# Optimization experiments

Measured on AMD Instinct MI355X. Metric: run time of the kernel, lower is better.

The kernel has to match this reference:

```python
import jax, jax.numpy as jnp
import numpy as np

N_NODES = 100000


def _gcn_conv(x, w, b, edge_index, n):
    # Linear transform
    x = x @ w + b
    # Add self loops
    loops = jnp.tile(jnp.arange(n, dtype=edge_index.dtype), (2, 1))
    ei = jnp.concatenate([edge_index, loops], axis=1)
    src, tgt = ei[0], ei[1]
    # Degree of source nodes (every node has a self loop -> deg >= 1)
    deg = jax.ops.segment_sum(jnp.ones(src.shape, x.dtype), src, num_segments=n)
    dinv = deg ** -0.5
    norm = dinv[src] * dinv[tgt]  # [E+N]
    # Gather-scale-scatter: out[t] += norm_e * x[s]
    msgs = norm[:, None] * x[src]  # [E+N, out_ch]
    return jax.ops.segment_sum(msgs, tgt, num_segments=n)


def setup_inputs() -> dict:
    key = jax.random.key(0)
    ks = jax.random.split(key, 6)
    n, f_in, hid, n_cls, e = N_NODES, 512, 16, 40, 3200000
    x = jax.random.normal(ks[0], (n, f_in), dtype=jnp.float32)
    edge_index = jax.random.randint(ks[1], (2, e), 0, n, dtype=jnp.int64)
    w1 = jax.random.normal(ks[2], (f_in, hid), dtype=jnp.float32) * (1.0 / np.sqrt(f_in))
    b1 = jax.random.normal(ks[3], (hid,), dtype=jnp.float32) * 0.01
    w2 = jax.random.normal(ks[4], (hid, n_cls), dtype=jnp.float32) * (1.0 / np.sqrt(hid))
    b2 = jax.random.normal(ks[5], (n_cls,), dtype=jnp.float32) * 0.01
    return {"x": x, "edge_index": edge_index, "w1": w1, "b1": b1, "w2": w2, "b2": b2}


def reference(x, edge_index, w1, b1, w2, b2):
    n = x.shape[0]
    h = _gcn_conv(x, w1, b1, edge_index, n)
    h = jax.nn.relu(h)
    # dropout is identity in eval mode (F.dropout with training=False)
    h = _gcn_conv(h, w2, b2, edge_index, n)
    return jax.nn.log_softmax(h, axis=1)
```

## Files before the change

### kernel.cpp

```cpp
#include <hip/hip_runtime.h>
#include <hip/hip_fp16.h>
#include <cstdint>

#define FIN 512
#define HID 16
#define NCLS 40
#define SHIFT 8
#define NBCAP 512
#define NBLK 512
#define BR 128
#define KC 32


__global__ void count_kernel(const int* __restrict__ ei, int E, int nb,
                             int* __restrict__ hist_src_g, int* __restrict__ hist_tgt_g) {
    __shared__ int hs[NBCAP], ht[NBCAP];
    for (int j = threadIdx.x; j < NBCAP; j += 256) { hs[j] = 0; ht[j] = 0; }
    __syncthreads();
    for (int i = blockIdx.x * 256 + threadIdx.x; i < E; i += NBLK * 256) {
        atomicAdd(&hs[ei[i] >> SHIFT], 1);
        atomicAdd(&ht[ei[E + i] >> SHIFT], 1);
    }
    __syncthreads();
    int base = blockIdx.x * NBCAP;
    for (int j = threadIdx.x; j < NBCAP; j += 256) {
        hist_src_g[base + j] = hs[j];
        hist_tgt_g[base + j] = ht[j];
    }
}


__global__ void colscan_kernel(int* __restrict__ hist_src_g, int* __restrict__ hist_tgt_g,
                               int* __restrict__ btot) {
    __shared__ int tmp[NBLK];
    int b = blockIdx.x;
    int* h = blockIdx.y ? hist_tgt_g : hist_src_g;
    int t = threadIdx.x;
    int v = h[t * NBCAP + b];
    tmp[t] = v;
    __syncthreads();
    for (int off = 1; off < NBLK; off <<= 1) {
        int a = (t >= off) ? tmp[t - off] : 0;
        __syncthreads();
        tmp[t] += a;
        __syncthreads();
    }
    h[t * NBCAP + b] = tmp[t] - v;
    if (t == NBLK - 1) btot[blockIdx.y * NBCAP + b] = tmp[NBLK - 1];
}


__global__ void bucketscan_kernel(const int* __restrict__ btot, int nb,
                                  int* __restrict__ src_base, int* __restrict__ tgt_base,
                                  int* __restrict__ row_ptr, int N, int E) {
    __shared__ int tmp[512];
    int t = threadIdx.x;
    int v = (t < nb) ? btot[t] : 0;
    tmp[t] = v;
    __syncthreads();
    for (int off = 1; off < 512; off <<= 1) {
        int a = (t >= off) ? tmp[t - off] : 0;
        __syncthreads();
        tmp[t] += a;
        __syncthreads();
    }
    if (t < nb) src_base[t] = tmp[t] - v;
    __syncthreads();
    int v2 = (t < nb) ? btot[NBCAP + t] : 0;
    tmp[t] = v2;
    __syncthreads();
    for (int off = 1; off < 512; off <<= 1) {
        int a = (t >= off) ? tmp[t - off] : 0;
        __syncthreads();
        tmp[t] += a;
        __syncthreads();
    }
    if (t < nb) tgt_base[t] = tmp[t] - v2;
    if (t == 0) { src_base[nb] = E; tgt_base[nb] = E; row_ptr[N] = E; }
}


__global__ void scatter_kernel(const int* __restrict__ ei, int E, int nb,
                               const int* __restrict__ hist_src_g,
                               const int* __restrict__ hist_tgt_g,
                               const int* __restrict__ src_base,
                               const int* __restrict__ tgt_base,
                               unsigned char* __restrict__ tmp_src,
                               unsigned int* __restrict__ tmp_tgt) {
    __shared__ int cs[NBCAP], ct[NBCAP];
    int blk = blockIdx.x;
    for (int j = threadIdx.x; j < nb; j += 256) {
        cs[j] = src_base[j] + hist_src_g[blk * NBCAP + j];
        ct[j] = tgt_base[j] + hist_tgt_g[blk * NBCAP + j];
    }
    __syncthreads();
    for (int i = blk * 256 + threadIdx.x; i < E; i += NBLK * 256) {
        int s = ei[i], tg = ei[E + i];
        int ps = atomicAdd(&cs[s >> SHIFT], 1);
        tmp_src[ps] = (unsigned char)(s & 255);
        int pt = atomicAdd(&ct[tg >> SHIFT], 1);
        tmp_tgt[pt] = ((unsigned int)(tg & 255) << 17) | (unsigned int)s;
    }
}


__global__ void finedeg_kernel(const unsigned char* __restrict__ tmp_src,
                               const int* __restrict__ src_base,
                               float* __restrict__ dinv, int N) {
    __shared__ int hist[256];
    int b = blockIdx.x;
    int t = threadIdx.x;
    hist[t] = 0;
    __syncthreads();
    int beg = src_base[b], end = src_base[b + 1];
    for (int i = beg + t; i < end; i += 256)
        atomicAdd(&hist[tmp_src[i]], 1);
    __syncthreads();
    int node = b * 256 + t;
    if (node < N) dinv[node] = rsqrtf((float)(hist[t] + 1));
}


__global__ void finecsr_kernel(const unsigned int* __restrict__ tmp_tgt,
                               const int* __restrict__ tgt_base,
                               const float* __restrict__ dinv,
                               int* __restrict__ row_ptr, int* __restrict__ edges,
                               __half* __restrict__ edinv, int N) {
    __shared__ int hist[256];
    __shared__ int scan[256];
    int b = blockIdx.x;
    int t = threadIdx.x;
    hist[t] = 0;
    __syncthreads();
    int beg = tgt_base[b], end = tgt_base[b + 1];
    for (int i = beg + t; i < end; i += 256)
        atomicAdd(&hist[tmp_tgt[i] >> 17], 1);
    __syncthreads();
    int v = hist[t];
    scan[t] = v;
    __syncthreads();
    for (int off = 1; off < 256; off <<= 1) {
        int a = (t >= off) ? scan[t - off] : 0;
        __syncthreads();
        scan[t] += a;
        __syncthreads();
    }
    int ex = scan[t] - v;
    int node = b * 256 + t;
    if (node < N) row_ptr[node] = beg + ex;
    hist[t] = ex;
    __syncthreads();
    for (int i = beg + t; i < end; i += 256) {
        unsigned int w = tmp_tgt[i];
        int tl = (int)(w >> 17);
        int src = (int)(w & 0x1FFFF);
        int pos = beg + atomicAdd(&hist[tl], 1);
        edges[pos] = src;
        edinv[pos] = __float2half(dinv[src]);
    }
}


__global__ void linear1_kernel(const float* __restrict__ x, const float* __restrict__ w1,
                               const float* __restrict__ b1, __half* __restrict__ h1h, int n) {
    __shared__ float xs[KC][BR + 2];
    __shared__ float wsc[KC * HID];
    __shared__ float bl[HID];
    int t = threadIdx.x;
    if (t < HID) bl[t] = b1[t];
    int row0 = blockIdx.x * BR;
    int rp = t >> 2;
    int cq = (t & 3) * 4;
    float acc0[4] = {0, 0, 0, 0};
    float acc1[4] = {0, 0, 0, 0};

    float4 xp[4];
    float wp[2];
    int rr_[4], kk_[4];
#pragma unroll
    for (int u = 0; u < 4; ++u) {
        int i = t + u * 256;
        rr_[u] = i >> 3;
        kk_[u] = (i & 7) * 4;
    }
    auto prefetch = [&](int kc) {
#pragma unroll
        for (int u = 0; u < 4; ++u) {
            int grow = row0 + rr_[u];
            xp[u] = (grow < n) ? *(const float4*)(x + (size_t)grow * FIN + kc + kk_[u])
                               : make_float4(0.f, 0.f, 0.f, 0.f);
        }
        wp[0] = w1[kc * HID + t];
        wp[1] = w1[kc * HID + t + 256];
    };

    prefetch(0);
    for (int kc = 0; kc < FIN; kc += KC) {
        __syncthreads();
#pragma unroll
        for (int u = 0; u < 4; ++u) {
            xs[kk_[u] + 0][rr_[u]] = xp[u].x;
            xs[kk_[u] + 1][rr_[u]] = xp[u].y;
            xs[kk_[u] + 2][rr_[u]] = xp[u].z;
            xs[kk_[u] + 3][rr_[u]] = xp[u].w;
        }
        wsc[t] = wp[0];
        wsc[t + 256] = wp[1];
        __syncthreads();
        if (kc + KC < FIN) prefetch(kc + KC);
#pragma unroll 8
        for (int k = 0; k < KC; ++k) {
            float2 xv = *(const float2*)&xs[k][2 * rp];
            float4 wv = *(const float4*)&wsc[k * HID + cq];
            acc0[0] = fmaf(xv.x, wv.x, acc0[0]);
            acc0[1] = fmaf(xv.x, wv.y, acc0[1]);
            acc0[2] = fmaf(xv.x, wv.z, acc0[2]);
            acc0[3] = fmaf(xv.x, wv.w, acc0[3]);
            acc1[0] = fmaf(xv.y, wv.x, acc1[0]);
            acc1[1] = fmaf(xv.y, wv.y, acc1[1]);
            acc1[2] = fmaf(xv.y, wv.z, acc1[2]);
            acc1[3] = fmaf(xv.y, wv.w, acc1[3]);
        }
    }
    int r0 = row0 + 2 * rp;
    if (r0 < n) {
        __half2* hp = (__half2*)(h1h + (size_t)r0 * HID + cq);
        hp[0] = __floats2half2_rn(acc0[0] + bl[cq + 0], acc0[1] + bl[cq + 1]);
        hp[1] = __floats2half2_rn(acc0[2] + bl[cq + 2], acc0[3] + bl[cq + 3]);
    }
    if (r0 + 1 < n) {
        __half2* hp = (__half2*)(h1h + (size_t)(r0 + 1) * HID + cq);
        hp[0] = __floats2half2_rn(acc1[0] + bl[cq + 0], acc1[1] + bl[cq + 1]);
        hp[1] = __floats2half2_rn(acc1[2] + bl[cq + 2], acc1[3] + bl[cq + 3]);
    }
}


__global__ void agg1_kernel(const __half* __restrict__ in, const int* __restrict__ edges,
                            const __half* __restrict__ edinv, const int* __restrict__ row_ptr,
                            const float* __restrict__ dinv, __half* __restrict__ out16,
                            float* __restrict__ rowsum, int n) {
    int gid = blockIdx.x * blockDim.x + threadIdx.x;
    int node = gid >> 4;
    int sub = (gid >> 3) & 1;
    int c2 = gid & 7;
    if (node >= n) return;
    const __half2* tab = (const __half2*)in;
    float dv = dinv[node];
    float self = dv * dv;
    float a0 = 0.f, a1 = 0.f, rs = 0.f;
    if (sub == 0) {
        float2 sv = __half22float2(tab[(size_t)node * 8 + c2]);
        a0 = self * sv.x; a1 = self * sv.y; rs = self;
    }
    int beg = row_ptr[node], end = row_ptr[node + 1];
#pragma unroll 4
    for (int i = beg + sub; i < end; i += 2) {
        int src = edges[i];
        float nrm = __half2float(edinv[i]) * dv;
        float2 v = __half22float2(tab[(size_t)src * 8 + c2]);
        a0 = fmaf(nrm, v.x, a0);
        a1 = fmaf(nrm, v.y, a1);
        rs += nrm;
    }
    a0 += __shfl_xor(a0, 8);
    a1 += __shfl_xor(a1, 8);
    rs += __shfl_xor(rs, 8);
    if (sub == 0) {
        a0 = fmaxf(a0, 0.f); a1 = fmaxf(a1, 0.f);
        ((__half2*)out16)[(size_t)node * 8 + c2] = __floats2half2_rn(a0, a1);
        if (c2 == 0) rowsum[node] = rs;
    }
}


__global__ void agg2_kernel(const __half* __restrict__ in, const int* __restrict__ edges,
                            const __half* __restrict__ edinv, const int* __restrict__ row_ptr,
                            const float* __restrict__ dinv, const float* __restrict__ rowsum,
                            const float* __restrict__ w2, const float* __restrict__ b2,
                            float* __restrict__ out, int n) {
    __shared__ float g2[16][HID + 1];
    __shared__ float wl[HID * NCLS];
    __shared__ float bl[NCLS];
    int t = threadIdx.x;
    for (int i = t; i < HID * NCLS; i += 256) wl[i] = w2[i];
    if (t < NCLS) bl[t] = b2[t];
    int gid = blockIdx.x * 256 + t;
    int node = gid >> 4;
    int sub = (t >> 3) & 1;
    int c2 = t & 7;
    int nl = t >> 4;
    float a0 = 0.f, a1 = 0.f;
    if (node < n) {
        const __half2* tab = (const __half2*)in;
        float dv = dinv[node];
        float self = dv * dv;
        if (sub == 0) {
            float2 sv = __half22float2(tab[(size_t)node * 8 + c2]);
            a0 = self * sv.x; a1 = self * sv.y;
        }
        int beg = row_ptr[node], end = row_ptr[node + 1];
#pragma unroll 4
        for (int i = beg + sub; i < end; i += 2) {
            int src = edges[i];
            float nrm = __half2float(edinv[i]) * dv;
            float2 v = __half22float2(tab[(size_t)src * 8 + c2]);
            a0 = fmaf(nrm, v.x, a0);
            a1 = fmaf(nrm, v.y, a1);
        }
    }
    a0 += __shfl_xor(a0, 8);
    a1 += __shfl_xor(a1, 8);
    if (sub == 0) { g2[nl][c2 * 2] = a0; g2[nl][c2 * 2 + 1] = a1; }
    __syncthreads();
    if (t < 32) {
        int nl2 = t >> 1, half = t & 1;
        int node2 = blockIdx.x * 16 + nl2;
        float z[20];
        float m = -1e30f, se = 0.f, lse = 0.f;
        if (node2 < n) {
            float h[HID];
#pragma unroll
            for (int j = 0; j < HID; ++j) h[j] = g2[nl2][j];
            float rs = rowsum[node2];
            int c0 = half * 20;
#pragma unroll
            for (int c = 0; c < 20; ++c) {
                float s = rs * bl[c0 + c];
#pragma unroll
                for (int j = 0; j < HID; ++j) s = fmaf(h[j], wl[j * NCLS + c0 + c], s);
                z[c] = s;
            }
            m = z[0];
#pragma unroll
            for (int c = 1; c < 20; ++c) m = fmaxf(m, z[c]);
        }
        m = fmaxf(m, __shfl_xor(m, 1));
        if (node2 < n) {
#pragma unroll
            for (int c = 0; c < 20; ++c) se += __expf(z[c] - m);
        }
        se += __shfl_xor(se, 1);
        if (node2 < n) {
            lse = m + __logf(se);
            float* orow = out + (size_t)node2 * NCLS + half * 20;
#pragma unroll
            for (int c = 0; c < 20; ++c) orow[c] = z[c] - lse;
        }
    }
}


extern "C" void kernel_launch(void* const* d_in, const int* in_sizes, int n_in,
                              void* d_out, int out_size, void* d_ws, size_t ws_size,
                              hipStream_t stream) {
    const float* x  = (const float*)d_in[0];
    const int*   ei = (const int*)d_in[1];
    const float* w1 = (const float*)d_in[2];
    const float* b1 = (const float*)d_in[3];
    const float* w2 = (const float*)d_in[4];
    const float* b2 = (const float*)d_in[5];
    float* out = (float*)d_out;

    int N = in_sizes[0] / FIN;
    int E = in_sizes[1] / 2;
    int nb = (N + 255) >> SHIFT;

    char* p = (char*)d_ws;
    auto alloc = [&](size_t bytes) -> char* {
        char* r = p;
        p += (bytes + 255) / 256 * 256;
        return r;
    };
    int*   hist_src_g = (int*)alloc((size_t)NBLK * NBCAP * 4);
    int*   hist_tgt_g = (int*)alloc((size_t)NBLK * NBCAP * 4);
    int*   btot       = (int*)alloc((size_t)2 * NBCAP * 4);
    int*   src_base   = (int*)alloc((size_t)(nb + 1) * 4);
    int*   tgt_base   = (int*)alloc((size_t)(nb + 1) * 4);
    float* dinv       = (float*)alloc((size_t)N * 4);
    int*   row_ptr    = (int*)alloc((size_t)(N + 1) * 4);
    unsigned char* tmp_src = (unsigned char*)alloc((size_t)E);
    unsigned int*  tmp_tgt = (unsigned int*)alloc((size_t)E * 4);
    int*    edges     = (int*)alloc((size_t)E * 4);
    __half* edinv     = (__half*)alloc((size_t)E * 2);
    __half* h1h       = (__half*)alloc((size_t)N * HID * 2);
    __half* gh        = (__half*)alloc((size_t)N * HID * 2);
    float*  rowsum    = (float*)alloc((size_t)N * 4);

    count_kernel<<<NBLK, 256, 0, stream>>>(ei, E, nb, hist_src_g, hist_tgt_g);
    colscan_kernel<<<dim3(nb, 2), NBLK, 0, stream>>>(hist_src_g, hist_tgt_g, btot);
    bucketscan_kernel<<<1, 512, 0, stream>>>(btot, nb, src_base, tgt_base, row_ptr, N, E);
    scatter_kernel<<<NBLK, 256, 0, stream>>>(ei, E, nb, hist_src_g, hist_tgt_g,
                                             src_base, tgt_base, tmp_src, tmp_tgt);
    finedeg_kernel<<<nb, 256, 0, stream>>>(tmp_src, src_base, dinv, N);
    finecsr_kernel<<<nb, 256, 0, stream>>>(tmp_tgt, tgt_base, dinv, row_ptr, edges, edinv, N);
    linear1_kernel<<<(N + BR - 1) / BR, 256, 0, stream>>>(x, w1, b1, h1h, N);
    agg1_kernel<<<(N * 16 + 255) / 256, 256, 0, stream>>>(h1h, edges, edinv, row_ptr, dinv,
                                                          gh, rowsum, N);
    agg2_kernel<<<(N * 16 + 255) / 256, 256, 0, stream>>>(gh, edges, edinv, row_ptr, dinv,
                                                          rowsum, w2, b2, out, N);
}
```

Before: 546.6 us.

## Vectorize edge loads, fuse fine kernels, drop edinv, widen aggregation threads

Count and scatter kernels now read edges as 4-wide nontemporal vectors. The degree and CSR fine kernels become one kernel. The per-edge half-precision dinv array is removed, so aggregation looks up dinv[src] directly. Aggregation uses 32 threads per node instead of 16, and linear1 uses 64-row tiles with launch bounds. The net effect mixes less stored data with an extra random gather per edge and more threads per node.

```diff
diff --git a/kernel.cpp b/kernel.cpp
--- a/kernel.cpp
+++ b/kernel.cpp
@@ -8,8 +8,11 @@
 #define SHIFT 8
 #define NBCAP 512
 #define NBLK 512
-#define BR 128
+#define BR 64
 #define KC 32
+
+typedef int   iv4 __attribute__((ext_vector_type(4)));
+typedef float fv4 __attribute__((ext_vector_type(4)));
 
 
 __global__ void count_kernel(const int* __restrict__ ei, int E, int nb,
@@ -17,9 +20,23 @@
     __shared__ int hs[NBCAP], ht[NBCAP];
     for (int j = threadIdx.x; j < NBCAP; j += 256) { hs[j] = 0; ht[j] = 0; }
     __syncthreads();
-    for (int i = blockIdx.x * 256 + threadIdx.x; i < E; i += NBLK * 256) {
-        atomicAdd(&hs[ei[i] >> SHIFT], 1);
-        atomicAdd(&ht[ei[E + i] >> SHIFT], 1);
+    if ((E & 3) == 0) {
+        const iv4* s4 = (const iv4*)ei;
+        const iv4* t4 = (const iv4*)(ei + E);
+        int E4 = E >> 2;
+        for (int i = blockIdx.x * 256 + threadIdx.x; i < E4; i += NBLK * 256) {
+            iv4 s = __builtin_nontemporal_load(&s4[i]);
+            iv4 t = __builtin_nontemporal_load(&t4[i]);
+            atomicAdd(&hs[s.x >> SHIFT], 1); atomicAdd(&hs[s.y >> SHIFT], 1);
+            atomicAdd(&hs[s.z >> SHIFT], 1); atomicAdd(&hs[s.w >> SHIFT], 1);
+            atomicAdd(&ht[t.x >> SHIFT], 1); atomicAdd(&ht[t.y >> SHIFT], 1);
+            atomicAdd(&ht[t.z >> SHIFT], 1); atomicAdd(&ht[t.w >> SHIFT], 1);
+        }
+    } else {
+        for (int i = blockIdx.x * 256 + threadIdx.x; i < E; i += NBLK * 256) {
+            atomicAdd(&hs[ei[i] >> SHIFT], 1);
+            atomicAdd(&ht[ei[E + i] >> SHIFT], 1);
+        }
     }
     __syncthreads();
     int base = blockIdx.x * NBCAP;
@@ -94,44 +111,58 @@
         ct[j] = tgt_base[j] + hist_tgt_g[blk * NBCAP + j];
     }
     __syncthreads();
-    for (int i = blk * 256 + threadIdx.x; i < E; i += NBLK * 256) {
-        int s = ei[i], tg = ei[E + i];
-        int ps = atomicAdd(&cs[s >> SHIFT], 1);
-        tmp_src[ps] = (unsigned char)(s & 255);
-        int pt = atomicAdd(&ct[tg >> SHIFT], 1);
-        tmp_tgt[pt] = ((unsigned int)(tg & 255) << 17) | (unsigned int)s;
-    }
-}
-
-
-__global__ void finedeg_kernel(const unsigned char* __restrict__ tmp_src,
-                               const int* __restrict__ src_base,
-                               float* __restrict__ dinv, int N) {
-    __shared__ int hist[256];
-    int b = blockIdx.x;
-    int t = threadIdx.x;
-    hist[t] = 0;
-    __syncthreads();
-    int beg = src_base[b], end = src_base[b + 1];
-    for (int i = beg + t; i < end; i += 256)
-        atomicAdd(&hist[tmp_src[i]], 1);
-    __syncthreads();
-    int node = b * 256 + t;
-    if (node < N) dinv[node] = rsqrtf((float)(hist[t] + 1));
-}
-
-
-__global__ void finecsr_kernel(const unsigned int* __restrict__ tmp_tgt,
-                               const int* __restrict__ tgt_base,
-                               const float* __restrict__ dinv,
-                               int* __restrict__ row_ptr, int* __restrict__ edges,
-                               __half* __restrict__ edinv, int N) {
+    if ((E & 3) == 0) {
+        const iv4* s4 = (const iv4*)ei;
+        const iv4* t4 = (const iv4*)(ei + E);
+        int E4 = E >> 2;
+        for (int i = blk * 256 + threadIdx.x; i < E4; i += NBLK * 256) {
+            iv4 s = __builtin_nontemporal_load(&s4[i]);
+            iv4 t = __builtin_nontemporal_load(&t4[i]);
+            int p;
+            p = atomicAdd(&cs[s.x >> SHIFT], 1); tmp_src[p] = (unsigned char)(s.x & 255);
+            p = atomicAdd(&cs[s.y >> SHIFT], 1); tmp_src[p] = (unsigned char)(s.y & 255);
+            p = atomicAdd(&cs[s.z >> SHIFT], 1); tmp_src[p] = (unsigned char)(s.z & 255);
+            p = atomicAdd(&cs[s.w >> SHIFT], 1); tmp_src[p] = (unsigned char)(s.w & 255);
+            p = atomicAdd(&ct[t.x >> SHIFT], 1); tmp_tgt[p] = ((unsigned int)(t.x & 255) << 17) | (unsigned int)s.x;
+            p = atomicAdd(&ct[t.y >> SHIFT], 1); tmp_tgt[p] = ((unsigned int)(t.y & 255) << 17) | (unsigned int)s.y;
+            p = atomicAdd(&ct[t.z >> SHIFT], 1); tmp_tgt[p] = ((unsigned int)(t.z & 255) << 17) | (unsigned int)s.z;
+            p = atomicAdd(&ct[t.w >> SHIFT], 1); tmp_tgt[p] = ((unsigned int)(t.w & 255) << 17) | (unsigned int)s.w;
+        }
+    } else {
+        for (int i = blk * 256 + threadIdx.x; i < E; i += NBLK * 256) {
+            int s = ei[i], tg = ei[E + i];
+            int ps = atomicAdd(&cs[s >> SHIFT], 1);
+            tmp_src[ps] = (unsigned char)(s & 255);
+            int pt = atomicAdd(&ct[tg >> SHIFT], 1);
+            tmp_tgt[pt] = ((unsigned int)(tg & 255) << 17) | (unsigned int)s;
+        }
+    }
+}
+
+
+__global__ void fine_kernel(const unsigned char* __restrict__ tmp_src,
+                            const int* __restrict__ src_base,
+                            const unsigned int* __restrict__ tmp_tgt,
+                            const int* __restrict__ tgt_base,
+                            float* __restrict__ dinv, int* __restrict__ row_ptr,
+                            int* __restrict__ edges, int N) {
     __shared__ int hist[256];
     __shared__ int scan[256];
     int b = blockIdx.x;
     int t = threadIdx.x;
     hist[t] = 0;
     __syncthreads();
+    {
+        int beg = src_base[b], end = src_base[b + 1];
+        for (int i = beg + t; i < end; i += 256)
+            atomicAdd(&hist[tmp_src[i]], 1);
+    }
+    __syncthreads();
+    int node = b * 256 + t;
+    if (node < N) dinv[node] = rsqrtf((float)(hist[t] + 1));
+    __syncthreads();
+    hist[t] = 0;
+    __syncthreads();
     int beg = tgt_base[b], end = tgt_base[b + 1];
     for (int i = beg + t; i < end; i += 256)
         atomicAdd(&hist[tmp_tgt[i] >> 17], 1);
@@ -146,7 +177,6 @@
         __syncthreads();
     }
     int ex = scan[t] - v;
-    int node = b * 256 + t;
     if (node < N) row_ptr[node] = beg + ex;
     hist[t] = ex;
     __syncthreads();
@@ -156,13 +186,13 @@
         int src = (int)(w & 0x1FFFF);
         int pos = beg + atomicAdd(&hist[tl], 1);
         edges[pos] = src;
-        edinv[pos] = __float2half(dinv[src]);
-    }
-}
-
-
-__global__ void linear1_kernel(const float* __restrict__ x, const float* __restrict__ w1,
-                               const float* __restrict__ b1, __half* __restrict__ h1h, int n) {
+    }
+}
+
+
+__global__ __launch_bounds__(256, 4)
+void linear1_kernel(const float* __restrict__ x, const float* __restrict__ w1,
+                    const float* __restrict__ b1, __half* __restrict__ h1h, int n) {
     __shared__ float xs[KC][BR + 2];
     __shared__ float wsc[KC * HID];
     __shared__ float bl[HID];
@@ -171,24 +201,26 @@
     int row0 = blockIdx.x * BR;
     int rp = t >> 2;
     int cq = (t & 3) * 4;
-    float acc0[4] = {0, 0, 0, 0};
-    float acc1[4] = {0, 0, 0, 0};
-
-    float4 xp[4];
+    float acc[4] = {0, 0, 0, 0};
+
+    fv4 xp[2];
     float wp[2];
-    int rr_[4], kk_[4];
-#pragma unroll
-    for (int u = 0; u < 4; ++u) {
+    int rr_[2], kk_[2];
+#pragma unroll
+    for (int u = 0; u < 2; ++u) {
         int i = t + u * 256;
         rr_[u] = i >> 3;
         kk_[u] = (i & 7) * 4;
     }
     auto prefetch = [&](int kc) {
 #pragma unroll
-        for (int u = 0; u < 4; ++u) {
+        for (int u = 0; u < 2; ++u) {
             int grow = row0 + rr_[u];
-            xp[u] = (grow < n) ? *(const float4*)(x + (size_t)grow * FIN + kc + kk_[u])
-                               : make_float4(0.f, 0.f, 0.f, 0.f);
+            if (grow < n) {
+                xp[u] = __builtin_nontemporal_load((const fv4*)(x + (size_t)grow * FIN + kc + kk_[u]));
+            } else {
+                xp[u] = (fv4){0.f, 0.f, 0.f, 0.f};
+            }
         }
         wp[0] = w1[kc * HID + t];
         wp[1] = w1[kc * HID + t + 256];
@@ -198,7 +230,7 @@
     for (int kc = 0; kc < FIN; kc += KC) {
         __syncthreads();
 #pragma unroll
-        for (int u = 0; u < 4; ++u) {
+        for (int u = 0; u < 2; ++u) {
             xs[kk_[u] + 0][rr_[u]] = xp[u].x;
             xs[kk_[u] + 1][rr_[u]] = xp[u].y;
             xs[kk_[u] + 2][rr_[u]] = xp[u].z;
@@ -210,62 +242,51 @@
         if (kc + KC < FIN) prefetch(kc + KC);
 #pragma unroll 8
         for (int k = 0; k < KC; ++k) {
-            float2 xv = *(const float2*)&xs[k][2 * rp];
+            float xv = xs[k][rp];
             float4 wv = *(const float4*)&wsc[k * HID + cq];
-            acc0[0] = fmaf(xv.x, wv.x, acc0[0]);
-            acc0[1] = fmaf(xv.x, wv.y, acc0[1]);
-            acc0[2] = fmaf(xv.x, wv.z, acc0[2]);
-            acc0[3] = fmaf(xv.x, wv.w, acc0[3]);
-            acc1[0] = fmaf(xv.y, wv.x, acc1[0]);
-            acc1[1] = fmaf(xv.y, wv.y, acc1[1]);
-            acc1[2] = fmaf(xv.y, wv.z, acc1[2]);
-            acc1[3] = fmaf(xv.y, wv.w, acc1[3]);
-        }
-    }
-    int r0 = row0 + 2 * rp;
+            acc[0] = fmaf(xv, wv.x, acc[0]);
+            acc[1] = fmaf(xv, wv.y, acc[1]);
+            acc[2] = fmaf(xv, wv.z, acc[2]);
+            acc[3] = fmaf(xv, wv.w, acc[3]);
+        }
+    }
+    int r0 = row0 + rp;
     if (r0 < n) {
         __half2* hp = (__half2*)(h1h + (size_t)r0 * HID + cq);
-        hp[0] = __floats2half2_rn(acc0[0] + bl[cq + 0], acc0[1] + bl[cq + 1]);
-        hp[1] = __floats2half2_rn(acc0[2] + bl[cq + 2], acc0[3] + bl[cq + 3]);
-    }
-    if (r0 + 1 < n) {
-        __half2* hp = (__half2*)(h1h + (size_t)(r0 + 1) * HID + cq);
-        hp[0] = __floats2half2_rn(acc1[0] + bl[cq + 0], acc1[1] + bl[cq + 1]);
-        hp[1] = __floats2half2_rn(acc1[2] + bl[cq + 2], acc1[3] + bl[cq + 3]);
+        hp[0] = __floats2half2_rn(acc[0] + bl[cq + 0], acc[1] + bl[cq + 1]);
+        hp[1] = __floats2half2_rn(acc[2] + bl[cq + 2], acc[3] + bl[cq + 3]);
     }
 }
 
 
 __global__ void agg1_kernel(const __half* __restrict__ in, const int* __restrict__ edges,
-                            const __half* __restrict__ edinv, const int* __restrict__ row_ptr,
-                            const float* __restrict__ dinv, __half* __restrict__ out16,
-                            float* __restrict__ rowsum, int n) {
+                            const int* __restrict__ row_ptr, const float* __restrict__ dinv,
+                            __half* __restrict__ out16, float* __restrict__ rowsum, int n) {
     int gid = blockIdx.x * blockDim.x + threadIdx.x;
-    int node = gid >> 4;
-    int sub = (gid >> 3) & 1;
+    int node = gid >> 5;
+    int sub = (gid >> 3) & 3;
     int c2 = gid & 7;
     if (node >= n) return;
     const __half2* tab = (const __half2*)in;
     float dv = dinv[node];
-    float self = dv * dv;
     float a0 = 0.f, a1 = 0.f, rs = 0.f;
     if (sub == 0) {
+        float self = dv * dv;
         float2 sv = __half22float2(tab[(size_t)node * 8 + c2]);
         a0 = self * sv.x; a1 = self * sv.y; rs = self;
     }
     int beg = row_ptr[node], end = row_ptr[node + 1];
 #pragma unroll 4
-    for (int i = beg + sub; i < end; i += 2) {
+    for (int i = beg + sub; i < end; i += 4) {
         int src = edges[i];
-        float nrm = __half2float(edinv[i]) * dv;
+        float nrm = dinv[src] * dv;
         float2 v = __half22float2(tab[(size_t)src * 8 + c2]);
         a0 = fmaf(nrm, v.x, a0);
         a1 = fmaf(nrm, v.y, a1);
         rs += nrm;
     }
-    a0 += __shfl_xor(a0, 8);
-    a1 += __shfl_xor(a1, 8);
-    rs += __shfl_xor(rs, 8);
+    a0 += __shfl_xor(a0, 8);  a1 += __shfl_xor(a1, 8);  rs += __shfl_xor(rs, 8);
+    a0 += __shfl_xor(a0, 16); a1 += __shfl_xor(a1, 16); rs += __shfl_xor(rs, 16);
     if (sub == 0) {
         a0 = fmaxf(a0, 0.f); a1 = fmaxf(a1, 0.f);
         ((__half2*)out16)[(size_t)node * 8 + c2] = __floats2half2_rn(a0, a1);
@@ -275,49 +296,49 @@
 
 
 __global__ void agg2_kernel(const __half* __restrict__ in, const int* __restrict__ edges,
-                            const __half* __restrict__ edinv, const int* __restrict__ row_ptr,
-                            const float* __restrict__ dinv, const float* __restrict__ rowsum,
+                            const int* __restrict__ row_ptr, const float* __restrict__ dinv,
+                            const float* __restrict__ rowsum,
                             const float* __restrict__ w2, const float* __restrict__ b2,
                             float* __restrict__ out, int n) {
-    __shared__ float g2[16][HID + 1];
+    __shared__ float g2[8][HID + 1];
     __shared__ float wl[HID * NCLS];
     __shared__ float bl[NCLS];
     int t = threadIdx.x;
     for (int i = t; i < HID * NCLS; i += 256) wl[i] = w2[i];
     if (t < NCLS) bl[t] = b2[t];
     int gid = blockIdx.x * 256 + t;
-    int node = gid >> 4;
-    int sub = (t >> 3) & 1;
+    int node = gid >> 5;
+    int sub = (t >> 3) & 3;
     int c2 = t & 7;
-    int nl = t >> 4;
+    int nl = t >> 5;
     float a0 = 0.f, a1 = 0.f;
     if (node < n) {
         const __half2* tab = (const __half2*)in;
         float dv = dinv[node];
-        float self = dv * dv;
         if (sub == 0) {
+            float self = dv * dv;
             float2 sv = __half22float2(tab[(size_t)node * 8 + c2]);
             a0 = self * sv.x; a1 = self * sv.y;
         }
         int beg = row_ptr[node], end = row_ptr[node + 1];
 #pragma unroll 4
-        for (int i = beg + sub; i < end; i += 2) {
+        for (int i = beg + sub; i < end; i += 4) {
             int src = edges[i];
-            float nrm = __half2float(edinv[i]) * dv;
+            float nrm = dinv[src] * dv;
             float2 v = __half22float2(tab[(size_t)src * 8 + c2]);
             a0 = fmaf(nrm, v.x, a0);
             a1 = fmaf(nrm, v.y, a1);
         }
     }
-    a0 += __shfl_xor(a0, 8);
-    a1 += __shfl_xor(a1, 8);
+    a0 += __shfl_xor(a0, 8);  a1 += __shfl_xor(a1, 8);
+    a0 += __shfl_xor(a0, 16); a1 += __shfl_xor(a1, 16);
     if (sub == 0) { g2[nl][c2 * 2] = a0; g2[nl][c2 * 2 + 1] = a1; }
     __syncthreads();
-    if (t < 32) {
+    if (t < 16) {
         int nl2 = t >> 1, half = t & 1;
-        int node2 = blockIdx.x * 16 + nl2;
+        int node2 = blockIdx.x * 8 + nl2;
         float z[20];
-        float m = -1e30f, se = 0.f, lse = 0.f;
+        float m = -1e30f, se = 0.f;
         if (node2 < n) {
             float h[HID];
 #pragma unroll
@@ -342,7 +363,7 @@
         }
         se += __shfl_xor(se, 1);
         if (node2 < n) {
-            lse = m + __logf(se);
+            float lse = m + __logf(se);
             float* orow = out + (size_t)node2 * NCLS + half * 20;
 #pragma unroll
             for (int c = 0; c < 20; ++c) orow[c] = z[c] - lse;
@@ -382,7 +403,6 @@
     unsigned char* tmp_src = (unsigned char*)alloc((size_t)E);
     unsigned int*  tmp_tgt = (unsigned int*)alloc((size_t)E * 4);
     int*    edges     = (int*)alloc((size_t)E * 4);
-    __half* edinv     = (__half*)alloc((size_t)E * 2);
     __half* h1h       = (__half*)alloc((size_t)N * HID * 2);
     __half* gh        = (__half*)alloc((size_t)N * HID * 2);
     float*  rowsum    = (float*)alloc((size_t)N * 4);
@@ -392,11 +412,11 @@
     bucketscan_kernel<<<1, 512, 0, stream>>>(btot, nb, src_base, tgt_base, row_ptr, N, E);
     scatter_kernel<<<NBLK, 256, 0, stream>>>(ei, E, nb, hist_src_g, hist_tgt_g,
                                              src_base, tgt_base, tmp_src, tmp_tgt);
-    finedeg_kernel<<<nb, 256, 0, stream>>>(tmp_src, src_base, dinv, N);
-    finecsr_kernel<<<nb, 256, 0, stream>>>(tmp_tgt, tgt_base, dinv, row_ptr, edges, edinv, N);
+    fine_kernel<<<nb, 256, 0, stream>>>(tmp_src, src_base, tmp_tgt, tgt_base,
+                                        dinv, row_ptr, edges, N);
     linear1_kernel<<<(N + BR - 1) / BR, 256, 0, stream>>>(x, w1, b1, h1h, N);
-    agg1_kernel<<<(N * 16 + 255) / 256, 256, 0, stream>>>(h1h, edges, edinv, row_ptr, dinv,
+    agg1_kernel<<<(N * 32 + 255) / 256, 256, 0, stream>>>(h1h, edges, row_ptr, dinv,
                                                           gh, rowsum, N);
-    agg2_kernel<<<(N * 16 + 255) / 256, 256, 0, stream>>>(gh, edges, edinv, row_ptr, dinv,
+    agg2_kernel<<<(N * 32 + 255) / 256, 256, 0, stream>>>(gh, edges, row_ptr, dinv,
                                                           rowsum, w2, b2, out, N);
 }
```

After: 514.0 us. 1.06x faster.
